# Kernel tuning notes

Measured on AMD Instinct MI355X. Metric: run time of the kernel, lower is better.

Reference implementation:

```python
import jax, jax.numpy as jnp
import numpy as np
from jax import lax

B, S, H = 2, 1024, 1024   # batch, seq, hidden_size
I = 512                   # moe_intermediate_size
E = 16                    # num_experts
TOP_K = 8                 # num_experts_per_tok


def setup_inputs() -> dict:
    key = jax.random.key(0)
    ks = jax.random.split(key, 5)
    scale_h = 1.0 / np.sqrt(H)
    scale_i = 1.0 / np.sqrt(I)
    return {
        "hidden_states": jax.random.normal(ks[0], (B, S, H), dtype=jnp.float32),
        "gate_w": jax.random.normal(ks[1], (H, E), dtype=jnp.float32) * scale_h,   # router
        "w_gate": jax.random.normal(ks[2], (E, H, I), dtype=jnp.float32) * scale_h,
        "w_up":   jax.random.normal(ks[3], (E, H, I), dtype=jnp.float32) * scale_h,
        "w_down": jax.random.normal(ks[4], (E, I, H), dtype=jnp.float32) * scale_i,
    }


def reference(hidden_states, gate_w, w_gate, w_up, w_down):
    b, s, h = hidden_states.shape
    x = hidden_states.reshape(-1, h)                      # [T, H]
    T = x.shape[0]

    router_logits = x @ gate_w                            # [T, E]
    probs = jax.nn.softmax(router_logits.astype(jnp.float32), axis=-1)
    top_w, top_i = lax.top_k(probs, TOP_K)                # [T, K]
    top_w = top_w / jnp.sum(top_w, axis=-1, keepdims=True)  # norm_topk_prob
    top_w = top_w.astype(x.dtype)

    # Dense per-token combine weights [T, E]; zero for unselected experts
    combine = jnp.zeros((T, E), dtype=x.dtype)
    combine = combine.at[jnp.arange(T)[:, None], top_i].add(top_w)

    # Scan over experts: masked gated-MLP, weighted accumulate (exact math;
    # unselected tokens contribute with weight 0, matching index_add scatter).
    def expert_step(acc, ws):
        wg, wu, wd, ce = ws                               # ce: [T] combine weights
        hmid = jax.nn.silu(x @ wg) * (x @ wu)             # [T, I]
        return acc + (hmid @ wd) * ce[:, None], None

    out, _ = lax.scan(expert_step, jnp.zeros_like(x),
                      (w_gate, w_up, w_down, combine.T))
    return out.reshape(b, s, h), router_logits
```

## Files before the change

kernel.cpp:

```cpp
#include <hip/hip_runtime.h>

typedef __attribute__((ext_vector_type(8))) short bf16x8;
typedef __attribute__((ext_vector_type(4))) float f32x4;
typedef __attribute__((ext_vector_type(4))) unsigned short u16x4;


static __device__ __forceinline__ unsigned short f2bfu(float f) {
  union { float f; unsigned u; } v; v.f = f;
  return (unsigned short)((v.u + 0x7fffu + ((v.u >> 16) & 1u)) >> 16);
}

static __device__ __forceinline__ float bfu2f(unsigned short u) {
  union { unsigned u; float f; } v; v.u = ((unsigned)u) << 16; return v.f;
}

static __device__ __forceinline__ void gload_lds16(const void* g, void* l) {
  __builtin_amdgcn_global_load_lds(
      (const __attribute__((address_space(1))) unsigned int*)g,
      (__attribute__((address_space(3))) unsigned int*)l, 16, 0, 0);
}

__global__ __launch_bounds__(256) void k_cast_bf16(const float* __restrict__ in,
                                                   unsigned short* __restrict__ out) {
  int i = blockIdx.x * 256 + threadIdx.x;
  float4 v = ((const float4*)in)[i];
  u16x4 o = { f2bfu(v.x), f2bfu(v.y), f2bfu(v.z), f2bfu(v.w) };
  *(u16x4*)(out + (size_t)i * 4) = o;
}

__global__ __launch_bounds__(256) void k_transpose64(const float* __restrict__ in,
                                                     unsigned short* __restrict__ out,
                                                     int R, int C, int ostride, long eoff) {
  __shared__ float tile[64][65];
  int z = blockIdx.z;
  int c0 = blockIdx.x * 64, r0 = blockIdx.y * 64;
  const float* src = in + (size_t)z * R * C;
  unsigned short* dst = out + (size_t)z * eoff;
  int cc = (threadIdx.x & 15) * 4, rr = threadIdx.x >> 4;
#pragma unroll
  for (int i = 0; i < 4; ++i) {
    float4 v = *(const float4*)(src + (size_t)(r0 + rr + i * 16) * C + c0 + cc);
    tile[rr + i * 16][cc + 0] = v.x; tile[rr + i * 16][cc + 1] = v.y;
    tile[rr + i * 16][cc + 2] = v.z; tile[rr + i * 16][cc + 3] = v.w;
  }
  __syncthreads();
#pragma unroll
  for (int i = 0; i < 4; ++i) {
    int oc = rr + i * 16;
    u16x4 o = { f2bfu(tile[cc + 0][oc]), f2bfu(tile[cc + 1][oc]),
                f2bfu(tile[cc + 2][oc]), f2bfu(tile[cc + 3][oc]) };
    *(u16x4*)(dst + (size_t)(c0 + oc) * ostride + r0 + cc) = o;
  }
}

__global__ __launch_bounds__(64) void k_router(const float* __restrict__ x,
                                               const float* __restrict__ gw,
                                               float* __restrict__ combine,
                                               float* __restrict__ logits) {
  int t = blockIdx.x;
  int lane = threadIdx.x;
  const float* xr = x + (size_t)t * 1024;
  float acc[16];
#pragma unroll
  for (int e = 0; e < 16; ++e) acc[e] = 0.f;
  for (int h = lane; h < 1024; h += 64) {
    float xv = xr[h];
    const float4* gr = (const float4*)(gw + (size_t)h * 16);
#pragma unroll
    for (int q = 0; q < 4; ++q) {
      float4 g4 = gr[q];
      acc[q * 4 + 0] += xv * g4.x;
      acc[q * 4 + 1] += xv * g4.y;
      acc[q * 4 + 2] += xv * g4.z;
      acc[q * 4 + 3] += xv * g4.w;
    }
  }
#pragma unroll
  for (int e = 0; e < 16; ++e) {
#pragma unroll
    for (int off = 32; off > 0; off >>= 1)
      acc[e] += __shfl_xor(acc[e], off);
  }
  if (lane < 16) logits[(size_t)t * 16 + lane] = acc[lane];

  float m = acc[0];
#pragma unroll
  for (int e = 1; e < 16; ++e) m = fmaxf(m, acc[e]);
  unsigned sel = 0u;
  for (int k = 0; k < 8; ++k) {
    float best = -3.4e38f; int bi = 0;
#pragma unroll
    for (int e = 0; e < 16; ++e)
      if (!((sel >> e) & 1u) && acc[e] > best) { best = acc[e]; bi = e; }
    sel |= 1u << bi;
  }
  float s = 0.f;
#pragma unroll
  for (int e = 0; e < 16; ++e)
    if ((sel >> e) & 1u) s += expf(acc[e] - m);
  float inv = 1.f / s;
  if (lane < 16)
    combine[(size_t)t * 16 + lane] = ((sel >> lane) & 1u) ? expf(acc[lane] - m) * inv : 0.f;
}

__global__ __launch_bounds__(256) void k_scan(const float* __restrict__ combine,
                                              unsigned short* __restrict__ idxlist,
                                              int* __restrict__ tokslot,
                                              int* __restrict__ counts) {
  __shared__ int wsum[4];
  const int e = blockIdx.x;
  const int tid = threadIdx.x;
  const int lane = tid & 63, w = tid >> 6;
  const int t0 = tid * 8;
  int flags = 0, cnt = 0;
#pragma unroll
  for (int j = 0; j < 8; ++j) {
    float c = combine[(size_t)(t0 + j) * 16 + e];
    if (c != 0.f) { flags |= 1 << j; ++cnt; }
  }
  int scan = cnt;
#pragma unroll
  for (int off = 1; off < 64; off <<= 1) {
    int v = __shfl_up(scan, off);
    if (lane >= off) scan += v;
  }
  if (lane == 63) wsum[w] = scan;
  __syncthreads();
  int base = 0;
  for (int i = 0; i < w; ++i) base += wsum[i];
  int pos = base + scan - cnt;
  for (int j = 0; j < 8; ++j) {
    if ((flags >> j) & 1) {
      idxlist[e * 2048 + pos] = (unsigned short)(t0 + j);
      tokslot[(t0 + j) * 16 + e] = pos;
      ++pos;
    } else {
      tokslot[(t0 + j) * 16 + e] = -1;
    }
  }
  if (tid == 255) counts[e] = base + scan;
}

__global__ __launch_bounds__(64) void k_offsets(const int* __restrict__ counts,
                                                int* __restrict__ ebase) {
  int lane = threadIdx.x;
  int c = (lane < 16) ? counts[lane] : 0;
  int s = c;
#pragma unroll
  for (int off = 1; off < 16; off <<= 1) {
    int v = __shfl_up(s, off);
    if (lane >= off) s += v;
  }
  if (lane < 16) ebase[lane] = s - c;
}

__global__ __launch_bounds__(512) void k_gateup(const unsigned short* __restrict__ xb,
                                                const unsigned short* __restrict__ wgt,
                                                const unsigned short* __restrict__ wut,
                                                const unsigned short* __restrict__ idxlist,
                                                const int* __restrict__ counts,
                                                const int* __restrict__ ebase,
                                                unsigned short* __restrict__ midp) {
  const int lb = (int)(blockIdx.x & 7) * 128 + (int)(blockIdx.x >> 3);
  const int mt = lb & 7, it = (lb >> 3) & 7, e = lb >> 6;
  const int Ne = counts[e];
  const int m0 = mt * 256;
  if (m0 >= Ne) return;
  const int i0 = it * 64;

  __shared__ alignas(16) char lds[49152];

  const int tid = threadIdx.x;
  const int lane = tid & 63;
  const int w = tid >> 6;
  const int wm = (w >> 1) * 64;
  const int wn = (w & 1) * 32;
  const int gb = ebase[e];

  const int crow = lane >> 2;
  const int slog = (lane & 3) ^ ((crow >> 1) & 3);

  const unsigned short* wge = wgt + (size_t)e * (512 * 1024);
  const unsigned short* wue = wut + (size_t)e * (512 * 1024);

  const unsigned short* gsrc[3];
  int loff[3];
#pragma unroll
  for (int q = 0; q < 3; ++q) {
    int c = 3 * w + q;
    loff[q] = c * 1024;
    if (c < 16) {
      int slot = m0 + c * 16 + crow;
      slot = slot < Ne ? slot : Ne - 1;
      gsrc[q] = xb + (size_t)idxlist[e * 2048 + slot] * 1024 + slog * 8;
    } else if (c < 20) {
      gsrc[q] = wge + (size_t)(i0 + (c - 16) * 16 + crow) * 1024 + slog * 8;
    } else {
      gsrc[q] = wue + (size_t)(i0 + (c - 20) * 16 + crow) * 1024 + slog * 8;
    }
  }

  auto stage = [&](int buf, int k0) {
    char* base = lds + buf * 24576;
#pragma unroll
    for (int q = 0; q < 3; ++q)
      gload_lds16(gsrc[q] + k0, base + loff[q]);
  };

  const int r0 = lane & 15;
  const int gp16 = ((lane >> 4) ^ ((r0 >> 1) & 3)) << 4;
  const int aoff  = ((wm + r0) << 6) + gp16;
  const int bgoff = 16384 + ((wn + r0) << 6) + gp16;
  const int buoff = 20480 + ((wn + r0) << 6) + gp16;

  f32x4 accg[4][2], accu[4][2];
#pragma unroll
  for (int fm = 0; fm < 4; ++fm)
#pragma unroll
    for (int fn = 0; fn < 2; ++fn) {
      accg[fm][fn] = f32x4{0.f, 0.f, 0.f, 0.f};
      accu[fm][fn] = f32x4{0.f, 0.f, 0.f, 0.f};
    }

  stage(0, 0);
  stage(1, 32);
  for (int t = 0; t < 32; ++t) {
    const int cur = t & 1;
    if (t == 31) asm volatile("s_waitcnt vmcnt(0)" ::: "memory");
    else         asm volatile("s_waitcnt vmcnt(3)" ::: "memory");
    __builtin_amdgcn_s_barrier();
    const char* base = lds + cur * 24576;
    bf16x8 a[4], bg[2], bu[2];
#pragma unroll
    for (int fm = 0; fm < 4; ++fm) a[fm] = *(const bf16x8*)(base + aoff + fm * 1024);
#pragma unroll
    for (int fn = 0; fn < 2; ++fn) {
      bg[fn] = *(const bf16x8*)(base + bgoff + fn * 1024);
      bu[fn] = *(const bf16x8*)(base + buoff + fn * 1024);
    }
    asm volatile("s_waitcnt lgkmcnt(0)" ::: "memory");
    __builtin_amdgcn_sched_barrier(0);
    __builtin_amdgcn_s_barrier();
    if (t + 2 < 32) stage(cur, (t + 2) * 32);
    __builtin_amdgcn_s_setprio(1);
#pragma unroll
    for (int fm = 0; fm < 4; ++fm)
#pragma unroll
      for (int fn = 0; fn < 2; ++fn) {
        accg[fm][fn] = __builtin_amdgcn_mfma_f32_16x16x32_bf16(a[fm], bg[fn], accg[fm][fn], 0, 0, 0);
        accu[fm][fn] = __builtin_amdgcn_mfma_f32_16x16x32_bf16(a[fm], bu[fn], accu[fm][fn], 0, 0, 0);
      }
    __builtin_amdgcn_s_setprio(0);
  }

  const int gq = lane >> 4;
#pragma unroll
  for (int fm = 0; fm < 4; ++fm) {
#pragma unroll
    for (int jj = 0; jj < 4; ++jj) {
      int slot = m0 + wm + fm * 16 + gq * 4 + jj;
      if (slot >= Ne) continue;
#pragma unroll
      for (int fn = 0; fn < 2; ++fn) {
        float gv = accg[fm][fn][jj];
        float uv = accu[fm][fn][jj];
        float mv = gv / (1.f + __expf(-gv)) * uv;
        midp[(size_t)(gb + slot) * 512 + i0 + wn + fn * 16 + r0] = f2bfu(mv);
      }
    }
  }
}

__global__ __launch_bounds__(512) void k_down(const unsigned short* __restrict__ midp,
                                              const unsigned short* __restrict__ wdt2,
                                              const int* __restrict__ counts,
                                              const int* __restrict__ ebase,
                                              unsigned short* __restrict__ dpk) {
  const int lb = (int)(blockIdx.x & 7) * 256 + (int)(blockIdx.x >> 3);
  const int mt = lb & 7, ht = (lb >> 3) & 15, e = lb >> 7;
  const int Ne = counts[e];
  const int m0 = mt * 256;
  if (m0 >= Ne) return;
  const int h0 = ht * 64;

  __shared__ alignas(16) char lds[40960];

  const int tid = threadIdx.x;
  const int lane = tid & 63;
  const int w = tid >> 6;
  const int wm = (w >> 1) * 64;
  const int wn = (w & 1) * 32;
  const int gb = ebase[e];

  const int crow = lane >> 2;
  const int slog = (lane & 3) ^ ((crow >> 1) & 3);

  const unsigned short* bsrc = wdt2 + (size_t)e * (512 * 1024);

  const unsigned short* gsrcA[2];
  int loffA[2];
#pragma unroll
  for (int q = 0; q < 2; ++q) {
    int c = q * 8 + w;
    loffA[q] = c * 1024;
    int slot = m0 + c * 16 + crow;
    slot = slot < Ne ? slot : Ne - 1;
    gsrcA[q] = midp + (size_t)(gb + slot) * 512 + slog * 8;
  }
  const unsigned short* gsrcB = nullptr;
  int loffB = 0;
  if (w >= 4) {
    loffB = 16384 + (w - 4) * 1024;
    gsrcB = bsrc + (size_t)(h0 + (w - 4) * 16 + crow) * 512 + slog * 8;
  }

  auto stage = [&](int buf, int k0) {
    char* base = lds + buf * 20480;
#pragma unroll
    for (int q = 0; q < 2; ++q)
      gload_lds16(gsrcA[q] + k0, base + loffA[q]);
    if (gsrcB) gload_lds16(gsrcB + k0, base + loffB);
  };

  const int r0 = lane & 15;
  const int gp16 = ((lane >> 4) ^ ((r0 >> 1) & 3)) << 4;
  const int aoff = ((wm + r0) << 6) + gp16;
  const int boff = 16384 + ((wn + r0) << 6) + gp16;

  f32x4 acc[4][2];
#pragma unroll
  for (int fm = 0; fm < 4; ++fm)
#pragma unroll
    for (int fn = 0; fn < 2; ++fn) acc[fm][fn] = f32x4{0.f, 0.f, 0.f, 0.f};

  stage(0, 0);
  stage(1, 32);
  for (int t = 0; t < 16; ++t) {
    const int cur = t & 1;
    if (t == 15)       asm volatile("s_waitcnt vmcnt(0)" ::: "memory");
    else if (w >= 4)   asm volatile("s_waitcnt vmcnt(3)" ::: "memory");
    else               asm volatile("s_waitcnt vmcnt(2)" ::: "memory");
    __builtin_amdgcn_s_barrier();
    const char* base = lds + cur * 20480;
    bf16x8 a[4], b[2];
#pragma unroll
    for (int fm = 0; fm < 4; ++fm) a[fm] = *(const bf16x8*)(base + aoff + fm * 1024);
#pragma unroll
    for (int fn = 0; fn < 2; ++fn) b[fn] = *(const bf16x8*)(base + boff + fn * 1024);
    asm volatile("s_waitcnt lgkmcnt(0)" ::: "memory");
    __builtin_amdgcn_sched_barrier(0);
    __builtin_amdgcn_s_barrier();
    if (t + 2 < 16) stage(cur, (t + 2) * 32);
    __builtin_amdgcn_s_setprio(1);
#pragma unroll
    for (int fm = 0; fm < 4; ++fm)
#pragma unroll
      for (int fn = 0; fn < 2; ++fn)
        acc[fm][fn] = __builtin_amdgcn_mfma_f32_16x16x32_bf16(a[fm], b[fn], acc[fm][fn], 0, 0, 0);
    __builtin_amdgcn_s_setprio(0);
  }

  const int gq = lane >> 4;
#pragma unroll
  for (int fm = 0; fm < 4; ++fm)
#pragma unroll
    for (int jj = 0; jj < 4; ++jj) {
      int slot = m0 + wm + fm * 16 + gq * 4 + jj;
      if (slot >= Ne) continue;
#pragma unroll
      for (int fn = 0; fn < 2; ++fn)
        dpk[(size_t)(gb + slot) * 1024 + h0 + wn + fn * 16 + r0] = f2bfu(acc[fm][fn][jj]);
    }
}

__global__ __launch_bounds__(128) void k_combine(const unsigned short* __restrict__ dpk,
                                                 const int* __restrict__ tokslot,
                                                 const int* __restrict__ ebase,
                                                 const float* __restrict__ combine,
                                                 float* __restrict__ out) {
  __shared__ int gsl[16];
  __shared__ float cws[16];
  const int t = blockIdx.x;
  const int tid = threadIdx.x;
  if (tid < 16) {
    int sl = tokslot[t * 16 + tid];
    gsl[tid] = (sl >= 0) ? ebase[tid] + sl : -1;
    cws[tid] = combine[(size_t)t * 16 + tid];
  }
  __syncthreads();
  float av[8];
#pragma unroll
  for (int j = 0; j < 8; ++j) av[j] = 0.f;
#pragma unroll
  for (int e = 0; e < 16; ++e) {
    int g = gsl[e];
    if (g < 0) continue;
    float cw = cws[e];
    bf16x8 v = *(const bf16x8*)(dpk + (size_t)g * 1024 + tid * 8);
#pragma unroll
    for (int j = 0; j < 8; ++j) av[j] += cw * bfu2f((unsigned short)v[j]);
  }
  float4 lo = { av[0], av[1], av[2], av[3] };
  float4 hi = { av[4], av[5], av[6], av[7] };
  float4* op = (float4*)(out + (size_t)t * 1024 + tid * 8);
  op[0] = lo;
  op[1] = hi;
}

extern "C" void kernel_launch(void* const* d_in, const int* in_sizes, int n_in,
                              void* d_out, int out_size, void* d_ws, size_t ws_size,
                              hipStream_t stream) {
  const float* x   = (const float*)d_in[0];
  const float* gw  = (const float*)d_in[1];
  const float* wga = (const float*)d_in[2];
  const float* wup = (const float*)d_in[3];
  const float* wdo = (const float*)d_in[4];
  float* out = (float*)d_out;
  float* logits = out + (size_t)2048 * 1024;

  char* ws = (char*)d_ws;
  unsigned short* xb   = (unsigned short*)(ws + 0);
  unsigned short* wgt  = (unsigned short*)(ws + 4194304);
  unsigned short* wut  = (unsigned short*)(ws + 20971520);
  unsigned short* wdt2 = (unsigned short*)(ws + 37748736);
  unsigned short* midp = (unsigned short*)(ws + 54525952);
  float* combine       = (float*)(ws + 71303168);
  int* tokslot         = (int*)(ws + 71434240);
  unsigned short* idxl = (unsigned short*)(ws + 71565312);
  int* counts          = (int*)(ws + 71630848);
  int* ebase           = (int*)(ws + 71630912);
  unsigned short* dpk  = (unsigned short*)(ws + 4194304);

  k_cast_bf16<<<2048, 256, 0, stream>>>(x, xb);
  k_transpose64<<<dim3(8, 16, 16), 256, 0, stream>>>(wga, wgt, 1024, 512, 1024, 524288L);
  k_transpose64<<<dim3(8, 16, 16), 256, 0, stream>>>(wup, wut, 1024, 512, 1024, 524288L);
  k_transpose64<<<dim3(16, 8, 16), 256, 0, stream>>>(wdo, wdt2, 512, 1024, 512, 524288L);
  k_router<<<2048, 64, 0, stream>>>(x, gw, combine, logits);
  k_scan<<<16, 256, 0, stream>>>(combine, idxl, tokslot, counts);
  k_offsets<<<1, 64, 0, stream>>>(counts, ebase);
  k_gateup<<<1024, 512, 0, stream>>>(xb, wgt, wut, idxl, counts, ebase, midp);
  k_down<<<2048, 512, 0, stream>>>(midp, wdt2, counts, ebase, dpk);
  k_combine<<<2048, 128, 0, stream>>>(dpk, tokslot, ebase, combine, out);
}
```

Before: 151.9 us.

## Use 32x32 MFMA with larger tiles, compact work list, fuse preprocessing kernels

The gate/up and down GEMMs switch from 16x16x32 to 32x32x16 bf16 MFMA and get larger per-block tiles (128 intermediate columns for gate/up, 256 hidden columns for down), with LDS raised to 64KB. A compact (expert, m-tile) pair list built in k_offsets lets the grids cover only populated tiles instead of launching blocks that exit early. The three weight transposes merge into one launch, and the bf16 cast of x moves into the router kernel. Together these cut launch count, idle blocks and LDS traffic per FLOP. In exchange each block uses more registers and LDS, so occupancy drops and there are fewer, larger blocks, which may hurt load balance.

Result: slower. 198.4 us (+30.6%).

```diff
diff --git a/kernel.cpp b/kernel.cpp
--- a/kernel.cpp
+++ b/kernel.cpp
@@ -1,7 +1,7 @@
 #include <hip/hip_runtime.h>
 
 typedef __attribute__((ext_vector_type(8))) short bf16x8;
-typedef __attribute__((ext_vector_type(4))) float f32x4;
+typedef __attribute__((ext_vector_type(16))) float f32x16;
 typedef __attribute__((ext_vector_type(4))) unsigned short u16x4;
 
 
@@ -20,22 +20,22 @@
       (__attribute__((address_space(3))) unsigned int*)l, 16, 0, 0);
 }
 
-__global__ __launch_bounds__(256) void k_cast_bf16(const float* __restrict__ in,
-                                                   unsigned short* __restrict__ out) {
-  int i = blockIdx.x * 256 + threadIdx.x;
-  float4 v = ((const float4*)in)[i];
-  u16x4 o = { f2bfu(v.x), f2bfu(v.y), f2bfu(v.z), f2bfu(v.w) };
-  *(u16x4*)(out + (size_t)i * 4) = o;
-}
-
-__global__ __launch_bounds__(256) void k_transpose64(const float* __restrict__ in,
-                                                     unsigned short* __restrict__ out,
-                                                     int R, int C, int ostride, long eoff) {
+__global__ __launch_bounds__(256) void k_transall(const float* __restrict__ wga,
+                                                  const float* __restrict__ wup,
+                                                  const float* __restrict__ wdo,
+                                                  unsigned short* __restrict__ wgt,
+                                                  unsigned short* __restrict__ wut,
+                                                  unsigned short* __restrict__ wdt2) {
   __shared__ float tile[64][65];
-  int z = blockIdx.z;
+  const int z = blockIdx.z;
+  const float* src;
+  unsigned short* dst;
+  int R, C, ostride;
+  if (z < 16)      { src = wga + (size_t)z * 524288; dst = wgt + (size_t)z * 524288; R = 1024; C = 512; ostride = 1024; }
+  else if (z < 32) { src = wup + (size_t)(z-16) * 524288; dst = wut + (size_t)(z-16) * 524288; R = 1024; C = 512; ostride = 1024; }
+  else             { src = wdo + (size_t)(z-32) * 524288; dst = wdt2 + (size_t)(z-32) * 524288; R = 512; C = 1024; ostride = 512; }
   int c0 = blockIdx.x * 64, r0 = blockIdx.y * 64;
-  const float* src = in + (size_t)z * R * C;
-  unsigned short* dst = out + (size_t)z * eoff;
+  if (c0 >= C || r0 >= R) return;
   int cc = (threadIdx.x & 15) * 4, rr = threadIdx.x >> 4;
 #pragma unroll
   for (int i = 0; i < 4; ++i) {
@@ -56,15 +56,18 @@
 __global__ __launch_bounds__(64) void k_router(const float* __restrict__ x,
                                                const float* __restrict__ gw,
                                                float* __restrict__ combine,
-                                               float* __restrict__ logits) {
+                                               float* __restrict__ logits,
+                                               unsigned short* __restrict__ xb) {
   int t = blockIdx.x;
   int lane = threadIdx.x;
   const float* xr = x + (size_t)t * 1024;
+  unsigned short* xbr = xb + (size_t)t * 1024;
   float acc[16];
 #pragma unroll
   for (int e = 0; e < 16; ++e) acc[e] = 0.f;
   for (int h = lane; h < 1024; h += 64) {
     float xv = xr[h];
+    xbr[h] = f2bfu(xv);
     const float4* gr = (const float4*)(gw + (size_t)h * 16);
 #pragma unroll
     for (int q = 0; q < 4; ++q) {
@@ -142,7 +145,9 @@
 }
 
 __global__ __launch_bounds__(64) void k_offsets(const int* __restrict__ counts,
-                                                int* __restrict__ ebase) {
+                                                int* __restrict__ ebase,
+                                                int* __restrict__ pairs,
+                                                int* __restrict__ pM) {
   int lane = threadIdx.x;
   int c = (lane < 16) ? counts[lane] : 0;
   int s = c;
@@ -152,6 +157,18 @@
     if (lane >= off) s += v;
   }
   if (lane < 16) ebase[lane] = s - c;
+  int nt = (lane < 16) ? ((c + 255) >> 8) : 0;
+  int ts = nt;
+#pragma unroll
+  for (int off = 1; off < 16; off <<= 1) {
+    int v = __shfl_up(ts, off);
+    if (lane >= off) ts += v;
+  }
+  if (lane < 16) {
+    int tb = ts - nt;
+    for (int j = 0; j < nt; ++j) pairs[tb + j] = (lane << 3) | j;
+  }
+  if (lane == 15) pM[0] = ts;
 }
 
 __global__ __launch_bounds__(512) void k_gateup(const unsigned short* __restrict__ xb,
@@ -160,21 +177,24 @@
                                                 const unsigned short* __restrict__ idxlist,
                                                 const int* __restrict__ counts,
                                                 const int* __restrict__ ebase,
+                                                const int* __restrict__ pairs,
+                                                const int* __restrict__ pM,
                                                 unsigned short* __restrict__ midp) {
-  const int lb = (int)(blockIdx.x & 7) * 128 + (int)(blockIdx.x >> 3);
-  const int mt = lb & 7, it = (lb >> 3) & 7, e = lb >> 6;
+  const int lb = (int)(blockIdx.x & 7) * 64 + (int)(blockIdx.x >> 3);
+  const int p = lb & 127, it = lb >> 7;
+  if (p >= pM[0]) return;
+  const int e = pairs[p] >> 3, mt = pairs[p] & 7;
   const int Ne = counts[e];
   const int m0 = mt * 256;
-  if (m0 >= Ne) return;
-  const int i0 = it * 64;
-
-  __shared__ alignas(16) char lds[49152];
+  const int i0 = it * 128;
+
+  __shared__ alignas(16) char lds[65536];
 
   const int tid = threadIdx.x;
   const int lane = tid & 63;
   const int w = tid >> 6;
-  const int wm = (w >> 1) * 64;
-  const int wn = (w & 1) * 32;
+  const int wm = (w & 3) * 64;
+  const int wn = (w >> 2) * 64;
   const int gb = ebase[e];
 
   const int crow = lane >> 2;
@@ -183,43 +203,51 @@
   const unsigned short* wge = wgt + (size_t)e * (512 * 1024);
   const unsigned short* wue = wut + (size_t)e * (512 * 1024);
 
-  const unsigned short* gsrc[3];
-  int loff[3];
-#pragma unroll
-  for (int q = 0; q < 3; ++q) {
-    int c = 3 * w + q;
+  const unsigned short* gsrc[4];
+  int loff[4];
+#pragma unroll
+  for (int q = 0; q < 4; ++q) {
+    int c = w * 4 + q;
     loff[q] = c * 1024;
     if (c < 16) {
       int slot = m0 + c * 16 + crow;
       slot = slot < Ne ? slot : Ne - 1;
       gsrc[q] = xb + (size_t)idxlist[e * 2048 + slot] * 1024 + slog * 8;
-    } else if (c < 20) {
+    } else if (c < 24) {
       gsrc[q] = wge + (size_t)(i0 + (c - 16) * 16 + crow) * 1024 + slog * 8;
     } else {
-      gsrc[q] = wue + (size_t)(i0 + (c - 20) * 16 + crow) * 1024 + slog * 8;
+      gsrc[q] = wue + (size_t)(i0 + (c - 24) * 16 + crow) * 1024 + slog * 8;
     }
   }
 
   auto stage = [&](int buf, int k0) {
-    char* base = lds + buf * 24576;
-#pragma unroll
-    for (int q = 0; q < 3; ++q)
+    char* base = lds + buf * 32768;
+#pragma unroll
+    for (int q = 0; q < 4; ++q)
       gload_lds16(gsrc[q] + k0, base + loff[q]);
   };
 
-  const int r0 = lane & 15;
-  const int gp16 = ((lane >> 4) ^ ((r0 >> 1) & 3)) << 4;
-  const int aoff  = ((wm + r0) << 6) + gp16;
-  const int bgoff = 16384 + ((wn + r0) << 6) + gp16;
-  const int buoff = 20480 + ((wn + r0) << 6) + gp16;
-
-  f32x4 accg[4][2], accu[4][2];
-#pragma unroll
-  for (int fm = 0; fm < 4; ++fm)
-#pragma unroll
-    for (int fn = 0; fn < 2; ++fn) {
-      accg[fm][fn] = f32x4{0.f, 0.f, 0.f, 0.f};
-      accu[fm][fn] = f32x4{0.f, 0.f, 0.f, 0.f};
+  const int l31 = lane & 31, lh = lane >> 5;
+  int aoff[2][2], bgoff[2][2], buoff[2][2];
+#pragma unroll
+  for (int f = 0; f < 2; ++f)
+#pragma unroll
+    for (int kk = 0; kk < 2; ++kk) {
+      int rowA = wm + f * 32 + l31;
+      aoff[f][kk] = rowA * 64 + (((kk * 2 + lh) ^ ((rowA >> 1) & 3)) << 4);
+      int rowB = wn + f * 32 + l31;
+      int bo = rowB * 64 + (((kk * 2 + lh) ^ ((rowB >> 1) & 3)) << 4);
+      bgoff[f][kk] = 16384 + bo;
+      buoff[f][kk] = 24576 + bo;
+    }
+
+  f32x16 accg[2][2], accu[2][2];
+#pragma unroll
+  for (int f = 0; f < 2; ++f)
+#pragma unroll
+    for (int g = 0; g < 2; ++g) {
+      accg[f][g] = (f32x16)(0.f);
+      accu[f][g] = (f32x16)(0.f);
     }
 
   stage(0, 0);
@@ -227,69 +255,73 @@
   for (int t = 0; t < 32; ++t) {
     const int cur = t & 1;
     if (t == 31) asm volatile("s_waitcnt vmcnt(0)" ::: "memory");
-    else         asm volatile("s_waitcnt vmcnt(3)" ::: "memory");
+    else         asm volatile("s_waitcnt vmcnt(4)" ::: "memory");
     __builtin_amdgcn_s_barrier();
-    const char* base = lds + cur * 24576;
-    bf16x8 a[4], bg[2], bu[2];
-#pragma unroll
-    for (int fm = 0; fm < 4; ++fm) a[fm] = *(const bf16x8*)(base + aoff + fm * 1024);
-#pragma unroll
-    for (int fn = 0; fn < 2; ++fn) {
-      bg[fn] = *(const bf16x8*)(base + bgoff + fn * 1024);
-      bu[fn] = *(const bf16x8*)(base + buoff + fn * 1024);
-    }
+    const char* base = lds + cur * 32768;
+    bf16x8 a[2][2], bg[2][2], bu[2][2];
+#pragma unroll
+    for (int f = 0; f < 2; ++f)
+#pragma unroll
+      for (int kk = 0; kk < 2; ++kk) {
+        a[f][kk]  = *(const bf16x8*)(base + aoff[f][kk]);
+        bg[f][kk] = *(const bf16x8*)(base + bgoff[f][kk]);
+        bu[f][kk] = *(const bf16x8*)(base + buoff[f][kk]);
+      }
     asm volatile("s_waitcnt lgkmcnt(0)" ::: "memory");
     __builtin_amdgcn_sched_barrier(0);
     __builtin_amdgcn_s_barrier();
     if (t + 2 < 32) stage(cur, (t + 2) * 32);
     __builtin_amdgcn_s_setprio(1);
 #pragma unroll
-    for (int fm = 0; fm < 4; ++fm)
-#pragma unroll
-      for (int fn = 0; fn < 2; ++fn) {
-        accg[fm][fn] = __builtin_amdgcn_mfma_f32_16x16x32_bf16(a[fm], bg[fn], accg[fm][fn], 0, 0, 0);
-        accu[fm][fn] = __builtin_amdgcn_mfma_f32_16x16x32_bf16(a[fm], bu[fn], accu[fm][fn], 0, 0, 0);
+    for (int kk = 0; kk < 2; ++kk)
+#pragma unroll
+      for (int f = 0; f < 2; ++f)
+#pragma unroll
+        for (int g = 0; g < 2; ++g) {
+          accg[f][g] = __builtin_amdgcn_mfma_f32_32x32x16_bf16(a[f][kk], bg[g][kk], accg[f][g], 0, 0, 0);
+          accu[f][g] = __builtin_amdgcn_mfma_f32_32x32x16_bf16(a[f][kk], bu[g][kk], accu[f][g], 0, 0, 0);
+        }
+    __builtin_amdgcn_s_setprio(0);
+  }
+
+#pragma unroll
+  for (int f = 0; f < 2; ++f)
+#pragma unroll
+    for (int g = 0; g < 2; ++g)
+#pragma unroll
+      for (int r = 0; r < 16; ++r) {
+        int rif = (r & 3) + 8 * (r >> 2) + 4 * lh;
+        int slot = m0 + wm + f * 32 + rif;
+        if (slot >= Ne) continue;
+        float gv = accg[f][g][r];
+        float uv = accu[f][g][r];
+        float mv = gv / (1.f + __expf(-gv)) * uv;
+        midp[(size_t)(gb + slot) * 512 + i0 + wn + g * 32 + l31] = f2bfu(mv);
       }
-    __builtin_amdgcn_s_setprio(0);
-  }
-
-  const int gq = lane >> 4;
-#pragma unroll
-  for (int fm = 0; fm < 4; ++fm) {
-#pragma unroll
-    for (int jj = 0; jj < 4; ++jj) {
-      int slot = m0 + wm + fm * 16 + gq * 4 + jj;
-      if (slot >= Ne) continue;
-#pragma unroll
-      for (int fn = 0; fn < 2; ++fn) {
-        float gv = accg[fm][fn][jj];
-        float uv = accu[fm][fn][jj];
-        float mv = gv / (1.f + __expf(-gv)) * uv;
-        midp[(size_t)(gb + slot) * 512 + i0 + wn + fn * 16 + r0] = f2bfu(mv);
-      }
-    }
-  }
 }
 
 __global__ __launch_bounds__(512) void k_down(const unsigned short* __restrict__ midp,
                                               const unsigned short* __restrict__ wdt2,
                                               const int* __restrict__ counts,
                                               const int* __restrict__ ebase,
+                                              const int* __restrict__ pairs,
+                                              const int* __restrict__ pM,
                                               unsigned short* __restrict__ dpk) {
-  const int lb = (int)(blockIdx.x & 7) * 256 + (int)(blockIdx.x >> 3);
-  const int mt = lb & 7, ht = (lb >> 3) & 15, e = lb >> 7;
+  const int lb = (int)(blockIdx.x & 7) * 64 + (int)(blockIdx.x >> 3);
+  const int p = lb & 127, ht = lb >> 7;
+  if (p >= pM[0]) return;
+  const int e = pairs[p] >> 3, mt = pairs[p] & 7;
   const int Ne = counts[e];
   const int m0 = mt * 256;
-  if (m0 >= Ne) return;
-  const int h0 = ht * 64;
-
-  __shared__ alignas(16) char lds[40960];
+  const int h0 = ht * 256;
+
+  __shared__ alignas(16) char lds[65536];
 
   const int tid = threadIdx.x;
   const int lane = tid & 63;
   const int w = tid >> 6;
-  const int wm = (w >> 1) * 64;
-  const int wn = (w & 1) * 32;
+  const int wm = (w & 1) * 128;
+  const int wn = (w >> 1) * 64;
   const int gb = ebase[e];
 
   const int crow = lane >> 2;
@@ -297,80 +329,96 @@
 
   const unsigned short* bsrc = wdt2 + (size_t)e * (512 * 1024);
 
-  const unsigned short* gsrcA[2];
-  int loffA[2];
-#pragma unroll
-  for (int q = 0; q < 2; ++q) {
-    int c = q * 8 + w;
-    loffA[q] = c * 1024;
-    int slot = m0 + c * 16 + crow;
-    slot = slot < Ne ? slot : Ne - 1;
-    gsrcA[q] = midp + (size_t)(gb + slot) * 512 + slog * 8;
-  }
-  const unsigned short* gsrcB = nullptr;
-  int loffB = 0;
-  if (w >= 4) {
-    loffB = 16384 + (w - 4) * 1024;
-    gsrcB = bsrc + (size_t)(h0 + (w - 4) * 16 + crow) * 512 + slog * 8;
+  const unsigned short* gsrc[4];
+  int loff[4];
+#pragma unroll
+  for (int q = 0; q < 4; ++q) {
+    int c = w * 4 + q;
+    loff[q] = c * 1024;
+    if (c < 16) {
+      int slot = m0 + c * 16 + crow;
+      slot = slot < Ne ? slot : Ne - 1;
+      gsrc[q] = midp + (size_t)(gb + slot) * 512 + slog * 8;
+    } else {
+      gsrc[q] = bsrc + (size_t)(h0 + (c - 16) * 16 + crow) * 512 + slog * 8;
+    }
   }
 
   auto stage = [&](int buf, int k0) {
-    char* base = lds + buf * 20480;
-#pragma unroll
-    for (int q = 0; q < 2; ++q)
-      gload_lds16(gsrcA[q] + k0, base + loffA[q]);
-    if (gsrcB) gload_lds16(gsrcB + k0, base + loffB);
+    char* base = lds + buf * 32768;
+#pragma unroll
+    for (int q = 0; q < 4; ++q)
+      gload_lds16(gsrc[q] + k0, base + loff[q]);
   };
 
-  const int r0 = lane & 15;
-  const int gp16 = ((lane >> 4) ^ ((r0 >> 1) & 3)) << 4;
-  const int aoff = ((wm + r0) << 6) + gp16;
-  const int boff = 16384 + ((wn + r0) << 6) + gp16;
-
-  f32x4 acc[4][2];
-#pragma unroll
-  for (int fm = 0; fm < 4; ++fm)
-#pragma unroll
-    for (int fn = 0; fn < 2; ++fn) acc[fm][fn] = f32x4{0.f, 0.f, 0.f, 0.f};
+  const int l31 = lane & 31, lh = lane >> 5;
+  int aoff[4][2], boff[2][2];
+#pragma unroll
+  for (int f = 0; f < 4; ++f)
+#pragma unroll
+    for (int kk = 0; kk < 2; ++kk) {
+      int rowA = wm + f * 32 + l31;
+      aoff[f][kk] = rowA * 64 + (((kk * 2 + lh) ^ ((rowA >> 1) & 3)) << 4);
+    }
+#pragma unroll
+  for (int g = 0; g < 2; ++g)
+#pragma unroll
+    for (int kk = 0; kk < 2; ++kk) {
+      int rowB = wn + g * 32 + l31;
+      boff[g][kk] = 16384 + rowB * 64 + (((kk * 2 + lh) ^ ((rowB >> 1) & 3)) << 4);
+    }
+
+  f32x16 acc[4][2];
+#pragma unroll
+  for (int f = 0; f < 4; ++f)
+#pragma unroll
+    for (int g = 0; g < 2; ++g) acc[f][g] = (f32x16)(0.f);
 
   stage(0, 0);
   stage(1, 32);
   for (int t = 0; t < 16; ++t) {
     const int cur = t & 1;
-    if (t == 15)       asm volatile("s_waitcnt vmcnt(0)" ::: "memory");
-    else if (w >= 4)   asm volatile("s_waitcnt vmcnt(3)" ::: "memory");
-    else               asm volatile("s_waitcnt vmcnt(2)" ::: "memory");
+    if (t == 15) asm volatile("s_waitcnt vmcnt(0)" ::: "memory");
+    else         asm volatile("s_waitcnt vmcnt(4)" ::: "memory");
     __builtin_amdgcn_s_barrier();
-    const char* base = lds + cur * 20480;
-    bf16x8 a[4], b[2];
-#pragma unroll
-    for (int fm = 0; fm < 4; ++fm) a[fm] = *(const bf16x8*)(base + aoff + fm * 1024);
-#pragma unroll
-    for (int fn = 0; fn < 2; ++fn) b[fn] = *(const bf16x8*)(base + boff + fn * 1024);
+    const char* base = lds + cur * 32768;
+    bf16x8 a[4][2], b[2][2];
+#pragma unroll
+    for (int f = 0; f < 4; ++f)
+#pragma unroll
+      for (int kk = 0; kk < 2; ++kk)
+        a[f][kk] = *(const bf16x8*)(base + aoff[f][kk]);
+#pragma unroll
+    for (int g = 0; g < 2; ++g)
+#pragma unroll
+      for (int kk = 0; kk < 2; ++kk)
+        b[g][kk] = *(const bf16x8*)(base + boff[g][kk]);
     asm volatile("s_waitcnt lgkmcnt(0)" ::: "memory");
     __builtin_amdgcn_sched_barrier(0);
     __builtin_amdgcn_s_barrier();
     if (t + 2 < 16) stage(cur, (t + 2) * 32);
     __builtin_amdgcn_s_setprio(1);
 #pragma unroll
-    for (int fm = 0; fm < 4; ++fm)
-#pragma unroll
-      for (int fn = 0; fn < 2; ++fn)
-        acc[fm][fn] = __builtin_amdgcn_mfma_f32_16x16x32_bf16(a[fm], b[fn], acc[fm][fn], 0, 0, 0);
+    for (int kk = 0; kk < 2; ++kk)
+#pragma unroll
+      for (int f = 0; f < 4; ++f)
+#pragma unroll
+        for (int g = 0; g < 2; ++g)
+          acc[f][g] = __builtin_amdgcn_mfma_f32_32x32x16_bf16(a[f][kk], b[g][kk], acc[f][g], 0, 0, 0);
     __builtin_amdgcn_s_setprio(0);
   }
 
-  const int gq = lane >> 4;
-#pragma unroll
-  for (int fm = 0; fm < 4; ++fm)
-#pragma unroll
-    for (int jj = 0; jj < 4; ++jj) {
-      int slot = m0 + wm + fm * 16 + gq * 4 + jj;
-      if (slot >= Ne) continue;
-#pragma unroll
-      for (int fn = 0; fn < 2; ++fn)
-        dpk[(size_t)(gb + slot) * 1024 + h0 + wn + fn * 16 + r0] = f2bfu(acc[fm][fn][jj]);
-    }
+#pragma unroll
+  for (int f = 0; f < 4; ++f)
+#pragma unroll
+    for (int g = 0; g < 2; ++g)
+#pragma unroll
+      for (int r = 0; r < 16; ++r) {
+        int rif = (r & 3) + 8 * (r >> 2) + 4 * lh;
+        int slot = m0 + wm + f * 32 + rif;
+        if (slot >= Ne) continue;
+        dpk[(size_t)(gb + slot) * 1024 + h0 + wn + g * 32 + l31] = f2bfu(acc[f][g][r]);
+      }
 }
 
 __global__ __launch_bounds__(128) void k_combine(const unsigned short* __restrict__ dpk,
@@ -429,16 +477,15 @@
   unsigned short* idxl = (unsigned short*)(ws + 71565312);
   int* counts          = (int*)(ws + 71630848);
   int* ebase           = (int*)(ws + 71630912);
+  int* pairs           = (int*)(ws + 71630976);
+  int* pM              = (int*)(ws + 71631488);
   unsigned short* dpk  = (unsigned short*)(ws + 4194304);
 
-  k_cast_bf16<<<2048, 256, 0, stream>>>(x, xb);
-  k_transpose64<<<dim3(8, 16, 16), 256, 0, stream>>>(wga, wgt, 1024, 512, 1024, 524288L);
-  k_transpose64<<<dim3(8, 16, 16), 256, 0, stream>>>(wup, wut, 1024, 512, 1024, 524288L);
-  k_transpose64<<<dim3(16, 8, 16), 256, 0, stream>>>(wdo, wdt2, 512, 1024, 512, 524288L);
-  k_router<<<2048, 64, 0, stream>>>(x, gw, combine, logits);
+  k_transall<<<dim3(16, 16, 48), 256, 0, stream>>>(wga, wup, wdo, wgt, wut, wdt2);
+  k_router<<<2048, 64, 0, stream>>>(x, gw, combine, logits, xb);
   k_scan<<<16, 256, 0, stream>>>(combine, idxl, tokslot, counts);
-  k_offsets<<<1, 64, 0, stream>>>(counts, ebase);
-  k_gateup<<<1024, 512, 0, stream>>>(xb, wgt, wut, idxl, counts, ebase, midp);
-  k_down<<<2048, 512, 0, stream>>>(midp, wdt2, counts, ebase, dpk);
+  k_offsets<<<1, 64, 0, stream>>>(counts, ebase, pairs, pM);
+  k_gateup<<<512, 512, 0, stream>>>(xb, wgt, wut, idxl, counts, ebase, pairs, pM, midp);
+  k_down<<<512, 512, 0, stream>>>(midp, wdt2, counts, ebase, pairs, pM, dpk);
   k_combine<<<2048, 128, 0, stream>>>(dpk, tokslot, ebase, combine, out);
 }
```

## Shrink MoE GEMM tiles, compact tile list, merge transposes and fold bf16 cast into router

Applied to the files above, without the earlier changes.

Merges the three weight transpose launches into one kernel and moves the activation bf16 cast into the router kernel, which removes launches and a separate pass over x. k_offsets now builds a compact list of (expert, 128-row tile) pairs. The gate-up and down kernels use 128-row tiles with 256 threads, indexed through that list, which cuts wasted blocks and padding from uneven expert counts and raises occupancy through smaller LDS. The cost is lower per-block reuse of weight tiles and more blocks that read the same weights.

Result: slower. 159.0 us (+4.6%).

```diff
diff --git a/kernel.cpp b/kernel.cpp
--- a/kernel.cpp
+++ b/kernel.cpp
@@ -20,22 +20,22 @@
       (__attribute__((address_space(3))) unsigned int*)l, 16, 0, 0);
 }
 
-__global__ __launch_bounds__(256) void k_cast_bf16(const float* __restrict__ in,
-                                                   unsigned short* __restrict__ out) {
-  int i = blockIdx.x * 256 + threadIdx.x;
-  float4 v = ((const float4*)in)[i];
-  u16x4 o = { f2bfu(v.x), f2bfu(v.y), f2bfu(v.z), f2bfu(v.w) };
-  *(u16x4*)(out + (size_t)i * 4) = o;
-}
-
-__global__ __launch_bounds__(256) void k_transpose64(const float* __restrict__ in,
-                                                     unsigned short* __restrict__ out,
-                                                     int R, int C, int ostride, long eoff) {
+__global__ __launch_bounds__(256) void k_transall(const float* __restrict__ wga,
+                                                  const float* __restrict__ wup,
+                                                  const float* __restrict__ wdo,
+                                                  unsigned short* __restrict__ wgt,
+                                                  unsigned short* __restrict__ wut,
+                                                  unsigned short* __restrict__ wdt2) {
   __shared__ float tile[64][65];
-  int z = blockIdx.z;
+  const int z = blockIdx.z;
+  const float* src;
+  unsigned short* dst;
+  int R, C, ostride;
+  if (z < 16)      { src = wga + (size_t)z * 524288; dst = wgt + (size_t)z * 524288; R = 1024; C = 512; ostride = 1024; }
+  else if (z < 32) { src = wup + (size_t)(z-16) * 524288; dst = wut + (size_t)(z-16) * 524288; R = 1024; C = 512; ostride = 1024; }
+  else             { src = wdo + (size_t)(z-32) * 524288; dst = wdt2 + (size_t)(z-32) * 524288; R = 512; C = 1024; ostride = 512; }
   int c0 = blockIdx.x * 64, r0 = blockIdx.y * 64;
-  const float* src = in + (size_t)z * R * C;
-  unsigned short* dst = out + (size_t)z * eoff;
+  if (c0 >= C || r0 >= R) return;
   int cc = (threadIdx.x & 15) * 4, rr = threadIdx.x >> 4;
 #pragma unroll
   for (int i = 0; i < 4; ++i) {
@@ -56,15 +56,18 @@
 __global__ __launch_bounds__(64) void k_router(const float* __restrict__ x,
                                                const float* __restrict__ gw,
                                                float* __restrict__ combine,
-                                               float* __restrict__ logits) {
+                                               float* __restrict__ logits,
+                                               unsigned short* __restrict__ xb) {
   int t = blockIdx.x;
   int lane = threadIdx.x;
   const float* xr = x + (size_t)t * 1024;
+  unsigned short* xbr = xb + (size_t)t * 1024;
   float acc[16];
 #pragma unroll
   for (int e = 0; e < 16; ++e) acc[e] = 0.f;
   for (int h = lane; h < 1024; h += 64) {
     float xv = xr[h];
+    xbr[h] = f2bfu(xv);
     const float4* gr = (const float4*)(gw + (size_t)h * 16);
 #pragma unroll
     for (int q = 0; q < 4; ++q) {
@@ -142,7 +145,9 @@
 }
 
 __global__ __launch_bounds__(64) void k_offsets(const int* __restrict__ counts,
-                                                int* __restrict__ ebase) {
+                                                int* __restrict__ ebase,
+                                                int* __restrict__ pairs,
+                                                int* __restrict__ pM) {
   int lane = threadIdx.x;
   int c = (lane < 16) ? counts[lane] : 0;
   int s = c;
@@ -152,23 +157,38 @@
     if (lane >= off) s += v;
   }
   if (lane < 16) ebase[lane] = s - c;
-}
-
-__global__ __launch_bounds__(512) void k_gateup(const unsigned short* __restrict__ xb,
+  int nt = (lane < 16) ? ((c + 127) >> 7) : 0;
+  int ts = nt;
+#pragma unroll
+  for (int off = 1; off < 16; off <<= 1) {
+    int v = __shfl_up(ts, off);
+    if (lane >= off) ts += v;
+  }
+  if (lane < 16) {
+    int tb = ts - nt;
+    for (int j = 0; j < nt; ++j) pairs[tb + j] = (lane << 4) | j;
+  }
+  if (lane == 15) pM[0] = ts;
+}
+
+__global__ __launch_bounds__(256) void k_gateup(const unsigned short* __restrict__ xb,
                                                 const unsigned short* __restrict__ wgt,
                                                 const unsigned short* __restrict__ wut,
                                                 const unsigned short* __restrict__ idxlist,
                                                 const int* __restrict__ counts,
                                                 const int* __restrict__ ebase,
+                                                const int* __restrict__ pairs,
+                                                const int* __restrict__ pM,
                                                 unsigned short* __restrict__ midp) {
-  const int lb = (int)(blockIdx.x & 7) * 128 + (int)(blockIdx.x >> 3);
-  const int mt = lb & 7, it = (lb >> 3) & 7, e = lb >> 6;
+  const int lb = (int)(blockIdx.x & 7) * 256 + (int)(blockIdx.x >> 3);
+  const int p = lb & 255, it = lb >> 8;
+  if (p >= pM[0]) return;
+  const int e = pairs[p] >> 4, mt = pairs[p] & 15;
   const int Ne = counts[e];
-  const int m0 = mt * 256;
-  if (m0 >= Ne) return;
+  const int m0 = mt * 128;
   const int i0 = it * 64;
 
-  __shared__ alignas(16) char lds[49152];
+  __shared__ alignas(16) char lds[32768];
 
   const int tid = threadIdx.x;
   const int lane = tid & 63;
@@ -183,35 +203,35 @@
   const unsigned short* wge = wgt + (size_t)e * (512 * 1024);
   const unsigned short* wue = wut + (size_t)e * (512 * 1024);
 
-  const unsigned short* gsrc[3];
-  int loff[3];
-#pragma unroll
-  for (int q = 0; q < 3; ++q) {
-    int c = 3 * w + q;
+  const unsigned short* gsrc[4];
+  int loff[4];
+#pragma unroll
+  for (int q = 0; q < 4; ++q) {
+    int c = w * 4 + q;
     loff[q] = c * 1024;
-    if (c < 16) {
+    if (c < 8) {
       int slot = m0 + c * 16 + crow;
       slot = slot < Ne ? slot : Ne - 1;
       gsrc[q] = xb + (size_t)idxlist[e * 2048 + slot] * 1024 + slog * 8;
-    } else if (c < 20) {
-      gsrc[q] = wge + (size_t)(i0 + (c - 16) * 16 + crow) * 1024 + slog * 8;
+    } else if (c < 12) {
+      gsrc[q] = wge + (size_t)(i0 + (c - 8) * 16 + crow) * 1024 + slog * 8;
     } else {
-      gsrc[q] = wue + (size_t)(i0 + (c - 20) * 16 + crow) * 1024 + slog * 8;
+      gsrc[q] = wue + (size_t)(i0 + (c - 12) * 16 + crow) * 1024 + slog * 8;
     }
   }
 
   auto stage = [&](int buf, int k0) {
-    char* base = lds + buf * 24576;
-#pragma unroll
-    for (int q = 0; q < 3; ++q)
+    char* base = lds + buf * 16384;
+#pragma unroll
+    for (int q = 0; q < 4; ++q)
       gload_lds16(gsrc[q] + k0, base + loff[q]);
   };
 
   const int r0 = lane & 15;
   const int gp16 = ((lane >> 4) ^ ((r0 >> 1) & 3)) << 4;
   const int aoff  = ((wm + r0) << 6) + gp16;
-  const int bgoff = 16384 + ((wn + r0) << 6) + gp16;
-  const int buoff = 20480 + ((wn + r0) << 6) + gp16;
+  const int bgoff = 8192  + ((wn + r0) << 6) + gp16;
+  const int buoff = 12288 + ((wn + r0) << 6) + gp16;
 
   f32x4 accg[4][2], accu[4][2];
 #pragma unroll
@@ -227,9 +247,9 @@
   for (int t = 0; t < 32; ++t) {
     const int cur = t & 1;
     if (t == 31) asm volatile("s_waitcnt vmcnt(0)" ::: "memory");
-    else         asm volatile("s_waitcnt vmcnt(3)" ::: "memory");
+    else         asm volatile("s_waitcnt vmcnt(4)" ::: "memory");
     __builtin_amdgcn_s_barrier();
-    const char* base = lds + cur * 24576;
+    const char* base = lds + cur * 16384;
     bf16x8 a[4], bg[2], bu[2];
 #pragma unroll
     for (int fm = 0; fm < 4; ++fm) a[fm] = *(const bf16x8*)(base + aoff + fm * 1024);
@@ -271,19 +291,22 @@
   }
 }
 
-__global__ __launch_bounds__(512) void k_down(const unsigned short* __restrict__ midp,
+__global__ __launch_bounds__(256) void k_down(const unsigned short* __restrict__ midp,
                                               const unsigned short* __restrict__ wdt2,
                                               const int* __restrict__ counts,
                                               const int* __restrict__ ebase,
+                                              const int* __restrict__ pairs,
+                                              const int* __restrict__ pM,
                                               unsigned short* __restrict__ dpk) {
-  const int lb = (int)(blockIdx.x & 7) * 256 + (int)(blockIdx.x >> 3);
-  const int mt = lb & 7, ht = (lb >> 3) & 15, e = lb >> 7;
+  const int lb = (int)(blockIdx.x & 7) * 512 + (int)(blockIdx.x >> 3);
+  const int p = lb & 255, ht = lb >> 8;
+  if (p >= pM[0]) return;
+  const int e = pairs[p] >> 4, mt = pairs[p] & 15;
   const int Ne = counts[e];
-  const int m0 = mt * 256;
-  if (m0 >= Ne) return;
+  const int m0 = mt * 128;
   const int h0 = ht * 64;
 
-  __shared__ alignas(16) char lds[40960];
+  __shared__ alignas(16) char lds[24576];
 
   const int tid = threadIdx.x;
   const int lane = tid & 63;
@@ -297,35 +320,32 @@
 
   const unsigned short* bsrc = wdt2 + (size_t)e * (512 * 1024);
 
-  const unsigned short* gsrcA[2];
-  int loffA[2];
-#pragma unroll
-  for (int q = 0; q < 2; ++q) {
-    int c = q * 8 + w;
-    loffA[q] = c * 1024;
-    int slot = m0 + c * 16 + crow;
-    slot = slot < Ne ? slot : Ne - 1;
-    gsrcA[q] = midp + (size_t)(gb + slot) * 512 + slog * 8;
-  }
-  const unsigned short* gsrcB = nullptr;
-  int loffB = 0;
-  if (w >= 4) {
-    loffB = 16384 + (w - 4) * 1024;
-    gsrcB = bsrc + (size_t)(h0 + (w - 4) * 16 + crow) * 512 + slog * 8;
+  const unsigned short* gsrc[3];
+  int loff[3];
+#pragma unroll
+  for (int q = 0; q < 3; ++q) {
+    int c = w * 3 + q;
+    loff[q] = c * 1024;
+    if (c < 8) {
+      int slot = m0 + c * 16 + crow;
+      slot = slot < Ne ? slot : Ne - 1;
+      gsrc[q] = midp + (size_t)(gb + slot) * 512 + slog * 8;
+    } else {
+      gsrc[q] = bsrc + (size_t)(h0 + (c - 8) * 16 + crow) * 512 + slog * 8;
+    }
   }
 
   auto stage = [&](int buf, int k0) {
-    char* base = lds + buf * 20480;
-#pragma unroll
-    for (int q = 0; q < 2; ++q)
-      gload_lds16(gsrcA[q] + k0, base + loffA[q]);
-    if (gsrcB) gload_lds16(gsrcB + k0, base + loffB);
+    char* base = lds + buf * 12288;
+#pragma unroll
+    for (int q = 0; q < 3; ++q)
+      gload_lds16(gsrc[q] + k0, base + loff[q]);
   };
 
   const int r0 = lane & 15;
   const int gp16 = ((lane >> 4) ^ ((r0 >> 1) & 3)) << 4;
   const int aoff = ((wm + r0) << 6) + gp16;
-  const int boff = 16384 + ((wn + r0) << 6) + gp16;
+  const int boff = 8192 + ((wn + r0) << 6) + gp16;
 
   f32x4 acc[4][2];
 #pragma unroll
@@ -337,11 +357,10 @@
   stage(1, 32);
   for (int t = 0; t < 16; ++t) {
     const int cur = t & 1;
-    if (t == 15)       asm volatile("s_waitcnt vmcnt(0)" ::: "memory");
-    else if (w >= 4)   asm volatile("s_waitcnt vmcnt(3)" ::: "memory");
-    else               asm volatile("s_waitcnt vmcnt(2)" ::: "memory");
+    if (t == 15) asm volatile("s_waitcnt vmcnt(0)" ::: "memory");
+    else         asm volatile("s_waitcnt vmcnt(3)" ::: "memory");
     __builtin_amdgcn_s_barrier();
-    const char* base = lds + cur * 20480;
+    const char* base = lds + cur * 12288;
     bf16x8 a[4], b[2];
 #pragma unroll
     for (int fm = 0; fm < 4; ++fm) a[fm] = *(const bf16x8*)(base + aoff + fm * 1024);
@@ -429,16 +448,15 @@
   unsigned short* idxl = (unsigned short*)(ws + 71565312);
   int* counts          = (int*)(ws + 71630848);
   int* ebase           = (int*)(ws + 71630912);
+  int* pairs           = (int*)(ws + 71630976);
+  int* pM              = (int*)(ws + 71632000);
   unsigned short* dpk  = (unsigned short*)(ws + 4194304);
 
-  k_cast_bf16<<<2048, 256, 0, stream>>>(x, xb);
-  k_transpose64<<<dim3(8, 16, 16), 256, 0, stream>>>(wga, wgt, 1024, 512, 1024, 524288L);
-  k_transpose64<<<dim3(8, 16, 16), 256, 0, stream>>>(wup, wut, 1024, 512, 1024, 524288L);
-  k_transpose64<<<dim3(16, 8, 16), 256, 0, stream>>>(wdo, wdt2, 512, 1024, 512, 524288L);
-  k_router<<<2048, 64, 0, stream>>>(x, gw, combine, logits);
+  k_transall<<<dim3(16, 16, 48), 256, 0, stream>>>(wga, wup, wdo, wgt, wut, wdt2);
+  k_router<<<2048, 64, 0, stream>>>(x, gw, combine, logits, xb);
   k_scan<<<16, 256, 0, stream>>>(combine, idxl, tokslot, counts);
-  k_offsets<<<1, 64, 0, stream>>>(counts, ebase);
-  k_gateup<<<1024, 512, 0, stream>>>(xb, wgt, wut, idxl, counts, ebase, midp);
-  k_down<<<2048, 512, 0, stream>>>(midp, wdt2, counts, ebase, dpk);
+  k_offsets<<<1, 64, 0, stream>>>(counts, ebase, pairs, pM);
+  k_gateup<<<2048, 256, 0, stream>>>(xb, wgt, wut, idxl, counts, ebase, pairs, pM, midp);
+  k_down<<<4096, 256, 0, stream>>>(midp, wdt2, counts, ebase, pairs, pM, dpk);
   k_combine<<<2048, 128, 0, stream>>>(dpk, tokslot, ebase, combine, out);
 }
```
